# Kernel optimization log

Hardware: AMD Instinct MI355X
Metric: run time of the kernel (lower is better)

The kernel has to match this reference:

```python
import jax, jax.numpy as jnp
import numpy as np

BIT_WIDTH = 4        # set via ol_update(bit_width, threshold) in the original
THRESHOLD = 0.997


def setup_inputs() -> dict:
    key = jax.random.key(0)
    x = jax.random.normal(key, (16, 2048, 2048), dtype=jnp.float32)
    return {"x": x}


def reference(x):
    # pos_only = False path: symmetric quantization over |x|
    n_lv_pos = 2 ** (BIT_WIDTH - 1) - 1  # 7 positive levels for 4-bit signed
    a = jnp.abs(x).reshape(-1)
    n = a.size
    nnz = jnp.sum(a != 0)
    # idx into ascending sort: skip the (n - nnz) zeros, then take the
    # THRESHOLD-quantile of the nonzero magnitudes (int() truncation as in torch)
    idx = jnp.floor(THRESHOLD * nnz.astype(jnp.float32)).astype(jnp.int32) + (n - nnz).astype(jnp.int32)
    idx = jnp.minimum(idx, n - 1)
    th_val = jnp.sort(a)[idx]
    # ol_quant_cuda: uniform quant for |x| <= th_val, outliers passed through
    step = th_val / n_lv_pos
    q = jnp.round(x / step) * step
    out = jnp.where(jnp.abs(x) <= th_val, q, x)
    # if th_val == 0 the original returns input unchanged
    return jnp.where(th_val > 0, out, x)
```

## Files before the change

### kernel.cpp

```cpp
#include <hip/hip_runtime.h>
#include <stdint.h>


#define COARSE_BITS 12
#define FINE_BITS   19
#define NCOARSE     (1u << COARSE_BITS)
#define NFINE       (1u << FINE_BITS)
#define NPART       256
#define CHUNK       (NFINE / NPART)

#define WS_CTRL   0
#define WS_COARSE 64
#define WS_FINE   4224
#define WS_PART   (WS_FINE + NFINE)
#define WS_WORDS  (WS_PART + NPART)

__global__ __launch_bounds__(256) void k_hist(const uint32_t* __restrict__ x,
                                              int n, uint32_t* __restrict__ ws) {
    __shared__ uint32_t h[NCOARSE];
    __shared__ uint32_t zc;
    for (int i = threadIdx.x; i < (int)NCOARSE; i += 256) h[i] = 0;
    if (threadIdx.x == 0) zc = 0;
    __syncthreads();

    const int n4 = n >> 2;
    const uint4* x4 = (const uint4*)x;
    const int stride = gridDim.x * blockDim.x;
    uint32_t myz = 0;
    for (int i = blockIdx.x * blockDim.x + threadIdx.x; i < n4; i += stride) {
        uint4 v = x4[i];
        uint32_t m0 = v.x & 0x7FFFFFFFu, m1 = v.y & 0x7FFFFFFFu;
        uint32_t m2 = v.z & 0x7FFFFFFFu, m3 = v.w & 0x7FFFFFFFu;
        atomicAdd(&h[m0 >> FINE_BITS], 1u);
        atomicAdd(&h[m1 >> FINE_BITS], 1u);
        atomicAdd(&h[m2 >> FINE_BITS], 1u);
        atomicAdd(&h[m3 >> FINE_BITS], 1u);
        myz += (m0 == 0u) + (m1 == 0u) + (m2 == 0u) + (m3 == 0u);
    }
    for (int i = (n4 << 2) + blockIdx.x * blockDim.x + threadIdx.x; i < n; i += stride) {
        uint32_t m = x[i] & 0x7FFFFFFFu;
        atomicAdd(&h[m >> FINE_BITS], 1u);
        myz += (m == 0u);
    }
    if (myz) atomicAdd(&zc, myz);
    __syncthreads();
    for (int i = threadIdx.x; i < (int)NCOARSE; i += 256) {
        uint32_t c = h[i];
        if (c) atomicAdd(&ws[WS_COARSE + i], c);
    }
    if (threadIdx.x == 0 && zc) atomicAdd(&ws[WS_CTRL + 4], zc);
}

__global__ __launch_bounds__(256) void k_select_coarse(uint32_t* __restrict__ ws, int n) {
    __shared__ uint32_t sums[256];
    __shared__ uint32_t ex[256];
    __shared__ uint32_t tgt;
    const int t = threadIdx.x;
    uint32_t local[16];
    uint32_t s = 0;
    for (int i = 0; i < 16; ++i) { local[i] = ws[WS_COARSE + t * 16 + i]; s += local[i]; }
    sums[t] = s;
    __syncthreads();
    if (t == 0) {
        uint32_t zeros = ws[WS_CTRL + 4];
        uint32_t nnz = (uint32_t)n - zeros;
        long long idx = (long long)floorf(0.997f * (float)nnz) + (long long)zeros;
        if (idx > (long long)n - 1) idx = (long long)n - 1;
        tgt = (uint32_t)idx;
        uint32_t run = 0;
        for (int i = 0; i < 256; ++i) { ex[i] = run; run += sums[i]; }
    }
    __syncthreads();
    const uint32_t r = tgt;
    if (r >= ex[t] && r < ex[t] + sums[t]) {
        uint32_t run = ex[t];
        for (int i = 0; i < 16; ++i) {
            if (r < run + local[i]) {
                ws[WS_CTRL + 0] = (uint32_t)(t * 16 + i);
                ws[WS_CTRL + 1] = r - run;
                break;
            }
            run += local[i];
        }
    }
}

__global__ __launch_bounds__(256) void k_fine(const uint32_t* __restrict__ x,
                                              int n, uint32_t* __restrict__ ws) {
    const uint32_t b = ws[WS_CTRL + 0];
    const int n4 = n >> 2;
    const uint4* x4 = (const uint4*)x;
    const int stride = gridDim.x * blockDim.x;
    for (int i = blockIdx.x * blockDim.x + threadIdx.x; i < n4; i += stride) {
        uint4 v = x4[i];
        uint32_t m;
        m = v.x & 0x7FFFFFFFu; if ((m >> FINE_BITS) == b) atomicAdd(&ws[WS_FINE + (m & (NFINE - 1u))], 1u);
        m = v.y & 0x7FFFFFFFu; if ((m >> FINE_BITS) == b) atomicAdd(&ws[WS_FINE + (m & (NFINE - 1u))], 1u);
        m = v.z & 0x7FFFFFFFu; if ((m >> FINE_BITS) == b) atomicAdd(&ws[WS_FINE + (m & (NFINE - 1u))], 1u);
        m = v.w & 0x7FFFFFFFu; if ((m >> FINE_BITS) == b) atomicAdd(&ws[WS_FINE + (m & (NFINE - 1u))], 1u);
    }
    for (int i = (n4 << 2) + blockIdx.x * blockDim.x + threadIdx.x; i < n; i += stride) {
        uint32_t m = x[i] & 0x7FFFFFFFu;
        if ((m >> FINE_BITS) == b) atomicAdd(&ws[WS_FINE + (m & (NFINE - 1u))], 1u);
    }
}

__global__ __launch_bounds__(256) void k_partials(uint32_t* __restrict__ ws) {
    __shared__ uint32_t red[256];
    const int t = threadIdx.x, j = blockIdx.x;
    uint32_t s = 0;
    for (int k = 0; k < CHUNK / 256; ++k) s += ws[WS_FINE + j * CHUNK + k * 256 + t];
    red[t] = s;
    __syncthreads();
    for (int o = 128; o > 0; o >>= 1) {
        if (t < o) red[t] += red[t + o];
        __syncthreads();
    }
    if (t == 0) ws[WS_PART + j] = red[0];
}

__global__ __launch_bounds__(256) void k_select_fine(uint32_t* __restrict__ ws) {
    __shared__ uint32_t sums[256];
    __shared__ uint32_t ex[256];
    __shared__ uint32_t chunk, r3;
    const int t = threadIdx.x;
    sums[t] = ws[WS_PART + t];
    __syncthreads();
    if (t == 0) {
        uint32_t r2 = ws[WS_CTRL + 1];
        uint32_t run = 0; int c = -1; uint32_t rr = 0;
        for (int i = 0; i < 256; ++i) {
            if (c < 0 && r2 < run + sums[i]) { c = i; rr = r2 - run; }
            run += sums[i];
        }
        chunk = (uint32_t)c;
        r3 = rr;
    }
    __syncthreads();
    const uint32_t c = chunk;
    uint32_t local[CHUNK / 256];
    uint32_t s = 0;
    for (int k = 0; k < CHUNK / 256; ++k) {
        local[k] = ws[WS_FINE + c * CHUNK + t * (CHUNK / 256) + k];
        s += local[k];
    }
    sums[t] = s;
    __syncthreads();
    if (t == 0) {
        uint32_t run = 0;
        for (int i = 0; i < 256; ++i) { ex[i] = run; run += sums[i]; }
    }
    __syncthreads();
    const uint32_t r = r3;
    if (r >= ex[t] && r < ex[t] + s) {
        uint32_t run = ex[t];
        for (int k = 0; k < CHUNK / 256; ++k) {
            if (r < run + local[k]) {
                uint32_t f = c * CHUNK + (uint32_t)t * (CHUNK / 256) + (uint32_t)k;
                uint32_t b = ws[WS_CTRL + 0];
                ws[WS_CTRL + 2] = (b << FINE_BITS) | f;
                break;
            }
            run += local[k];
        }
    }
}

__device__ __forceinline__ float ol_q(float v, float th, float step) {
    float q = rintf(v / step) * step;
    return (th > 0.0f && fabsf(v) <= th) ? q : v;
}

__global__ __launch_bounds__(256) void k_quant(const float* __restrict__ x,
                                               float* __restrict__ out,
                                               const uint32_t* __restrict__ ws, int n) {
    const float th = __uint_as_float(ws[WS_CTRL + 2]);
    const float step = th / 7.0f;
    const int n4 = n >> 2;
    const float4* x4 = (const float4*)x;
    float4* o4 = (float4*)out;
    const int stride = gridDim.x * blockDim.x;
    for (int i = blockIdx.x * blockDim.x + threadIdx.x; i < n4; i += stride) {
        float4 v = x4[i];
        float4 o;
        o.x = ol_q(v.x, th, step);
        o.y = ol_q(v.y, th, step);
        o.z = ol_q(v.z, th, step);
        o.w = ol_q(v.w, th, step);
        o4[i] = o;
    }
    for (int i = (n4 << 2) + blockIdx.x * blockDim.x + threadIdx.x; i < n; i += stride) {
        out[i] = ol_q(x[i], th, step);
    }
}

extern "C" void kernel_launch(void* const* d_in, const int* in_sizes, int n_in,
                              void* d_out, int out_size, void* d_ws, size_t ws_size,
                              hipStream_t stream) {
    const float* x = (const float*)d_in[0];
    const uint32_t* xb = (const uint32_t*)d_in[0];
    float* out = (float*)d_out;
    uint32_t* ws = (uint32_t*)d_ws;
    const int n = in_sizes[0];

    hipMemsetAsync(d_ws, 0, (size_t)WS_WORDS * sizeof(uint32_t), stream);

    const int blocks = 2048;
    k_hist<<<blocks, 256, 0, stream>>>(xb, n, ws);
    k_select_coarse<<<1, 256, 0, stream>>>(ws, n);
    k_fine<<<blocks, 256, 0, stream>>>(xb, n, ws);
    k_partials<<<NPART, 256, 0, stream>>>(ws);
    k_select_fine<<<1, 256, 0, stream>>>(ws);
    k_quant<<<blocks, 256, 0, stream>>>(x, out, ws, n);
}
```

Before: 564.3 us.

## Compact large-magnitude candidates during histogram pass to skip second full read

During the coarse histogram pass, each block also writes every magnitude at or above a fixed pivot (|x| >= 2.0) into a per-block candidate buffer. It does this with wave ballots and a shared counter. If the selected coarse bin lies above the pivot and no block overflowed its buffer, the fine histogram is built from the compacted candidates instead of rereading all 64M elements, and a full-scan fallback kernel covers the other cases. It also splits the shared coarse histogram into two copies to reduce atomic contention. The cost is extra ballot and shuffle work plus global writes in the first pass, and the fast path depends on the quantile landing above the pivot, which holds for normally distributed inputs.

Measured after the change: 537.7 us. 4.7% less time.

```diff
diff --git a/kernel.cpp b/kernel.cpp
--- a/kernel.cpp
+++ b/kernel.cpp
@@ -8,20 +8,29 @@
 #define NFINE       (1u << FINE_BITS)
 #define NPART       256
 #define CHUNK       (NFINE / NPART)
+#define NBLOCKS     2048
+#define CAP         4096
+#define PIVOT_BITS  0x40000000u
 
 #define WS_CTRL   0
 #define WS_COARSE 64
 #define WS_FINE   4224
 #define WS_PART   (WS_FINE + NFINE)
-#define WS_WORDS  (WS_PART + NPART)
-
-__global__ __launch_bounds__(256) void k_hist(const uint32_t* __restrict__ x,
-                                              int n, uint32_t* __restrict__ ws) {
-    __shared__ uint32_t h[NCOARSE];
-    __shared__ uint32_t zc;
-    for (int i = threadIdx.x; i < (int)NCOARSE; i += 256) h[i] = 0;
-    if (threadIdx.x == 0) zc = 0;
-    __syncthreads();
+#define WS_BCNT   (WS_PART + NPART)
+#define WS_ZERO_WORDS (WS_BCNT + NBLOCKS)
+#define WS_CAND   (WS_BCNT + NBLOCKS)
+
+__global__ __launch_bounds__(256) void k_histc(const uint32_t* __restrict__ x,
+                                               int n, uint32_t* __restrict__ ws) {
+    __shared__ uint32_t h[2][NCOARSE];
+    __shared__ uint32_t zc, bcnt;
+    for (int i = threadIdx.x; i < (int)NCOARSE; i += 256) { h[0][i] = 0; h[1][i] = 0; }
+    if (threadIdx.x == 0) { zc = 0; bcnt = 0; }
+    __syncthreads();
+
+    const int lane = threadIdx.x & 63;
+    uint32_t* hh = h[(threadIdx.x >> 6) & 1];
+    uint32_t* region = ws + WS_CAND + (size_t)blockIdx.x * CAP;
 
     const int n4 = n >> 2;
     const uint4* x4 = (const uint4*)x;
@@ -31,24 +40,49 @@
         uint4 v = x4[i];
         uint32_t m0 = v.x & 0x7FFFFFFFu, m1 = v.y & 0x7FFFFFFFu;
         uint32_t m2 = v.z & 0x7FFFFFFFu, m3 = v.w & 0x7FFFFFFFu;
-        atomicAdd(&h[m0 >> FINE_BITS], 1u);
-        atomicAdd(&h[m1 >> FINE_BITS], 1u);
-        atomicAdd(&h[m2 >> FINE_BITS], 1u);
-        atomicAdd(&h[m3 >> FINE_BITS], 1u);
+        atomicAdd(&hh[m0 >> FINE_BITS], 1u);
+        atomicAdd(&hh[m1 >> FINE_BITS], 1u);
+        atomicAdd(&hh[m2 >> FINE_BITS], 1u);
+        atomicAdd(&hh[m3 >> FINE_BITS], 1u);
         myz += (m0 == 0u) + (m1 == 0u) + (m2 == 0u) + (m3 == 0u);
+
+        unsigned long long b0 = __ballot(m0 >= PIVOT_BITS);
+        unsigned long long b1 = __ballot(m1 >= PIVOT_BITS);
+        unsigned long long b2 = __ballot(m2 >= PIVOT_BITS);
+        unsigned long long b3 = __ballot(m3 >= PIVOT_BITS);
+        uint32_t c0 = (uint32_t)__popcll(b0);
+        uint32_t c1 = (uint32_t)__popcll(b1);
+        uint32_t c2 = (uint32_t)__popcll(b2);
+        uint32_t c3 = (uint32_t)__popcll(b3);
+        uint32_t tot = c0 + c1 + c2 + c3;
+        if (tot) {
+            uint32_t wbase = 0;
+            if (lane == 0) wbase = atomicAdd(&bcnt, tot);
+            wbase = (uint32_t)__shfl((int)wbase, 0, 64);
+            unsigned long long lt = (1ULL << lane) - 1ULL;
+            if (m0 >= PIVOT_BITS) { uint32_t p = wbase + (uint32_t)__popcll(b0 & lt);                 if (p < CAP) region[p] = m0; }
+            if (m1 >= PIVOT_BITS) { uint32_t p = wbase + c0 + (uint32_t)__popcll(b1 & lt);            if (p < CAP) region[p] = m1; }
+            if (m2 >= PIVOT_BITS) { uint32_t p = wbase + c0 + c1 + (uint32_t)__popcll(b2 & lt);       if (p < CAP) region[p] = m2; }
+            if (m3 >= PIVOT_BITS) { uint32_t p = wbase + c0 + c1 + c2 + (uint32_t)__popcll(b3 & lt);  if (p < CAP) region[p] = m3; }
+        }
     }
     for (int i = (n4 << 2) + blockIdx.x * blockDim.x + threadIdx.x; i < n; i += stride) {
         uint32_t m = x[i] & 0x7FFFFFFFu;
-        atomicAdd(&h[m >> FINE_BITS], 1u);
+        atomicAdd(&hh[m >> FINE_BITS], 1u);
         myz += (m == 0u);
+        if (m >= PIVOT_BITS) { uint32_t p = atomicAdd(&bcnt, 1u); if (p < CAP) region[p] = m; }
     }
     if (myz) atomicAdd(&zc, myz);
     __syncthreads();
     for (int i = threadIdx.x; i < (int)NCOARSE; i += 256) {
-        uint32_t c = h[i];
+        uint32_t c = h[0][i] + h[1][i];
         if (c) atomicAdd(&ws[WS_COARSE + i], c);
     }
-    if (threadIdx.x == 0 && zc) atomicAdd(&ws[WS_CTRL + 4], zc);
+    if (threadIdx.x == 0) {
+        if (zc) atomicAdd(&ws[WS_CTRL + 4], zc);
+        ws[WS_BCNT + blockIdx.x] = bcnt;
+        if (bcnt > CAP) atomicOr(&ws[WS_CTRL + 5], 1u);
+    }
 }
 
 __global__ __launch_bounds__(256) void k_select_coarse(uint32_t* __restrict__ ws, int n) {
@@ -76,8 +110,10 @@
         uint32_t run = ex[t];
         for (int i = 0; i < 16; ++i) {
             if (r < run + local[i]) {
-                ws[WS_CTRL + 0] = (uint32_t)(t * 16 + i);
+                uint32_t b = (uint32_t)(t * 16 + i);
+                ws[WS_CTRL + 0] = b;
                 ws[WS_CTRL + 1] = r - run;
+                ws[WS_CTRL + 3] = (b >= (PIVOT_BITS >> FINE_BITS) && ws[WS_CTRL + 5] == 0u) ? 1u : 0u;
                 break;
             }
             run += local[i];
@@ -85,8 +121,21 @@
     }
 }
 
-__global__ __launch_bounds__(256) void k_fine(const uint32_t* __restrict__ x,
-                                              int n, uint32_t* __restrict__ ws) {
+__global__ __launch_bounds__(256) void k_fine_c(uint32_t* __restrict__ ws) {
+    if (ws[WS_CTRL + 3] == 0u) return;
+    const uint32_t b = ws[WS_CTRL + 0];
+    uint32_t cnt = ws[WS_BCNT + blockIdx.x];
+    if (cnt > CAP) cnt = CAP;
+    const uint32_t* region = ws + WS_CAND + (size_t)blockIdx.x * CAP;
+    for (uint32_t i = threadIdx.x; i < cnt; i += 256u) {
+        uint32_t m = region[i];
+        if ((m >> FINE_BITS) == b) atomicAdd(&ws[WS_FINE + (m & (NFINE - 1u))], 1u);
+    }
+}
+
+__global__ __launch_bounds__(256) void k_fine_full(const uint32_t* __restrict__ x,
+                                                   int n, uint32_t* __restrict__ ws) {
+    if (ws[WS_CTRL + 3] != 0u) return;
     const uint32_t b = ws[WS_CTRL + 0];
     const int n4 = n >> 2;
     const uint4* x4 = (const uint4*)x;
@@ -203,13 +252,13 @@
     uint32_t* ws = (uint32_t*)d_ws;
     const int n = in_sizes[0];
 
-    hipMemsetAsync(d_ws, 0, (size_t)WS_WORDS * sizeof(uint32_t), stream);
-
-    const int blocks = 2048;
-    k_hist<<<blocks, 256, 0, stream>>>(xb, n, ws);
+    hipMemsetAsync(d_ws, 0, (size_t)WS_ZERO_WORDS * sizeof(uint32_t), stream);
+
+    k_histc<<<NBLOCKS, 256, 0, stream>>>(xb, n, ws);
     k_select_coarse<<<1, 256, 0, stream>>>(ws, n);
-    k_fine<<<blocks, 256, 0, stream>>>(xb, n, ws);
+    k_fine_c<<<NBLOCKS, 256, 0, stream>>>(ws);
+    k_fine_full<<<NBLOCKS, 256, 0, stream>>>(xb, n, ws);
     k_partials<<<NPART, 256, 0, stream>>>(ws);
     k_select_fine<<<1, 256, 0, stream>>>(ws);
-    k_quant<<<blocks, 256, 0, stream>>>(x, out, ws, n);
-}
+    k_quant<<<NBLOCKS, 256, 0, stream>>>(x, out, ws, n);
+}
```
